# Kernel optimization log

Measured on AMD Instinct MI355X. Metric: run time of the kernel, lower is better.

The kernel has to match this reference:

```python
import jax, jax.numpy as jnp
import numpy as np

DIM = 256
HEADS = 8
HD = DIM // HEADS        # head_dim = 32
WS = 8                   # window_size (Wh = Ww = 8)
NEXP = 8                 # num_experts
HID = 128                # attr_hidden_size (router hidden)
SCALE = HD ** -0.5


def _window_partition(x, ws):
    # (B, H, W, C) -> (B * H//ws * W//ws, ws, ws, C)
    B, H, W, C = x.shape
    x = x.reshape(B, H // ws, ws, W // ws, ws, C)
    return x.transpose(0, 1, 3, 2, 4, 5).reshape(-1, ws, ws, C)


def _window_reverse(w, ws, B, H, W):
    # inverse of _window_partition
    C = w.shape[-1]
    x = w.reshape(B, H // ws, W // ws, ws, ws, C)
    return x.transpose(0, 1, 3, 2, 4, 5).reshape(B, H, W, C)


def _rope2(x):
    # 2D rotary embedding over a window: x (B*, Wh, Ww, d).
    # First d/2 channels rotated by row position, last d/2 by column position.
    B, Wh, Ww, d = x.shape
    d2 = d // 2

    def angles(L, dd):
        inv = 1.0 / (10000.0 ** (jnp.arange(0, dd, 2, dtype=jnp.float32) / dd))
        return jnp.arange(L, dtype=jnp.float32)[:, None] * inv[None, :]  # (L, dd//2)

    def rotate(v, ang, bshape):
        # v: (B, Wh, Ww, dd) pairs interleaved; ang broadcast as bshape
        p = v.reshape(*v.shape[:-1], -1, 2)
        c = jnp.cos(ang).reshape(bshape)
        s = jnp.sin(ang).reshape(bshape)
        o0 = p[..., 0] * c - p[..., 1] * s
        o1 = p[..., 0] * s + p[..., 1] * c
        return jnp.stack([o0, o1], axis=-1).reshape(v.shape)

    ah = angles(Wh, d2)  # (Wh, d2//2)
    aw = angles(Ww, d2)  # (Ww, d2//2)
    xh = rotate(x[..., :d2], ah, (1, Wh, 1, d2 // 2))
    xw = rotate(x[..., d2:], aw, (1, 1, Ww, d2 // 2))
    return jnp.concatenate([xh, xw], axis=-1)


def _moe_linear(xf, routes, w, b):
    # Top-1 dispatch: per-expert dense GEMM, masked select (jit-safe, static shapes).
    # xf: (T, in), routes: (T,) int, w: (E, out, in), b: (E, out)
    out = jnp.zeros((xf.shape[0], w.shape[1]), xf.dtype)
    for i in range(w.shape[0]):
        y = xf @ w[i].T + b[i]
        out = jnp.where((routes == i)[:, None], y, out)
    return out


def setup_inputs() -> dict:
    key = jax.random.key(0)
    ks = jax.random.split(key, 8)
    sc = 0.02
    return {
        "x": jax.random.normal(ks[0], (8, 64, 64, DIM), jnp.float32),
        "router_w1": jax.random.normal(ks[1], (HID, DIM), jnp.float32) * sc,
        "router_b1": jnp.zeros((HID,), jnp.float32),
        "router_w2": jax.random.normal(ks[2], (NEXP, HID), jnp.float32) * sc,
        "router_b2": jnp.zeros((NEXP,), jnp.float32),
        "qkv_w": jax.random.normal(ks[3], (NEXP, 3 * DIM, DIM), jnp.float32) * sc,
        "qkv_b": jnp.zeros((NEXP, 3 * DIM), jnp.float32),
        "proj_w": jax.random.normal(ks[4], (NEXP, DIM, DIM), jnp.float32) * sc,
        "proj_b": jnp.zeros((NEXP, DIM), jnp.float32),
    }


def reference(x, router_w1, router_b1, router_w2, router_b2,
              qkv_w, qkv_b, proj_w, proj_b):
    Bs, H, W, C = x.shape
    xf = x.reshape(-1, C)  # (T, C), T = Bs*H*W

    # --- Top-1 router (eval mode: no noise, no token dropping) ---
    h = jax.nn.relu(xf @ router_w1.T + router_b1)
    router_logits = h @ router_w2.T + router_b2          # (T, E)
    router_probs = jax.nn.softmax(router_logits, axis=-1)
    route_prob_max = jnp.max(router_probs, axis=-1)       # (T,)
    routes = jnp.argmax(router_probs, axis=-1)            # (T,)

    # --- per-expert QKV projection (grouped dispatch) ---
    qkv = _moe_linear(xf, routes, qkv_w, qkv_b)           # (T, 3C)
    qkv = qkv.reshape(Bs, H, W, 3 * C)

    # --- window partition (shift=0, dilated=1 -> no roll, mask=None) ---
    qw = _window_partition(qkv, WS).reshape(-1, WS * WS, 3 * C)
    B_, N, _ = qw.shape
    qkv5 = qw.reshape(B_, N, 3, HEADS, HD).transpose(2, 0, 3, 1, 4)  # (3,B_,h,N,hd)
    q, k, v = qkv5[0], qkv5[1], qkv5[2]

    # --- RoPE on q, k over the 2D window ---
    q = _rope2(q.reshape(-1, WS, WS, HD)).reshape(B_, HEADS, N, HD)
    k = _rope2(k.reshape(-1, WS, WS, HD)).reshape(B_, HEADS, N, HD)

    # --- windowed attention (moe_mask is all zeros in eval: no drops) ---
    attn = jax.nn.softmax((q * SCALE) @ k.swapaxes(-2, -1), axis=-1)  # (B_,h,N,N)
    out = (attn @ v).swapaxes(1, 2).reshape(B_, N, C)

    # --- window reverse ---
    out = _window_reverse(out.reshape(-1, WS, WS, C), WS, Bs, H, W)

    # --- per-expert output projection + Switch-style prob scaling ---
    of = _moe_linear(out.reshape(-1, C), routes, proj_w, proj_b)
    of = of * route_prob_max[:, None]
    return of.reshape(Bs, H, W, C)
```

## Files before the change

kernel.cpp:

```cpp
#include <hip/hip_runtime.h>
#include <hip/hip_bf16.h>

typedef unsigned short u16;
typedef unsigned int u32;
typedef __attribute__((ext_vector_type(8))) short short8;
typedef __attribute__((ext_vector_type(4))) float f32x4;

#define T_TOK 32768
#define SCALE_ATT 0.17677669529663687f

__device__ __forceinline__ u16 f2bf(float f){
  u32 u = __float_as_uint(f);
  u32 r = u + 0x7fffu + ((u >> 16) & 1u);
  return (u16)(r >> 16);
}
__device__ __forceinline__ float bf2f(u16 h){
  return __uint_as_float(((u32)h) << 16);
}

__global__ void k_cvt(const float* __restrict__ s, u16* __restrict__ d, int n4){
  int i = blockIdx.x * blockDim.x + threadIdx.x;
  if (i < n4){
    float4 v = ((const float4*)s)[i];
    ushort4 o;
    o.x = f2bf(v.x); o.y = f2bf(v.y); o.z = f2bf(v.z); o.w = f2bf(v.w);
    ((ushort4*)d)[i] = o;
  }
}

__global__ void k_cvt_split(const float* __restrict__ s, u16* __restrict__ hi,
                            u16* __restrict__ lo, int n){
  int i = blockIdx.x * blockDim.x + threadIdx.x;
  if (i < n){
    float v = s[i];
    u16 h = f2bf(v);
    hi[i] = h;
    lo[i] = f2bf(v - bf2f(h));
  }
}

__global__ void k_init(int* counts, int* cursors){
  int t = threadIdx.x;
  if (t < 8){ counts[t] = 0; cursors[t] = 0; }
}

__global__ __launch_bounds__(256) void k_router(
    const float* __restrict__ x, const u16* __restrict__ w1h, const u16* __restrict__ w1l,
    const float* __restrict__ b1, const float* __restrict__ w2, const float* __restrict__ b2,
    int* __restrict__ routes, float* __restrict__ pmax, int* __restrict__ counts,
    u16* __restrict__ x_bf)
{
  __shared__ __align__(16) char smem[64*132*4];
  u16* Ah = (u16*)smem;
  u16* Al = Ah + 2560;
  u16* Bh = Al + 2560;
  u16* Bl = Bh + 5120;
  float* Hs = (float*)smem;
  __shared__ int lhist[8];

  int tid = threadIdx.x;
  int t0 = blockIdx.x * 64;
  int wv = tid >> 6, lane = tid & 63, quad = lane >> 4, l16 = lane & 15;
  if (tid < 8) lhist[tid] = 0;

  int arow = tid >> 2, acg = tid & 3;
  int brow = tid >> 1, bhalf = tid & 1;

  f32x4 acc[4][2];
  #pragma unroll
  for (int i = 0; i < 4; ++i)
    #pragma unroll
    for (int j = 0; j < 2; ++j)
      #pragma unroll
      for (int rr = 0; rr < 4; ++rr) acc[i][j][rr] = 0.f;

  for (int kt = 0; kt < 8; ++kt){
    const float* gx = x + (size_t)(t0 + arow) * 256 + kt * 32 + acg * 8;
    float4 v0 = *(const float4*)gx;
    float4 v1 = *(const float4*)(gx + 4);
    ushort4 h0, h1, l0, l1;
    h0.x = f2bf(v0.x); h0.y = f2bf(v0.y); h0.z = f2bf(v0.z); h0.w = f2bf(v0.w);
    h1.x = f2bf(v1.x); h1.y = f2bf(v1.y); h1.z = f2bf(v1.z); h1.w = f2bf(v1.w);
    l0.x = f2bf(v0.x - bf2f(h0.x)); l0.y = f2bf(v0.y - bf2f(h0.y));
    l0.z = f2bf(v0.z - bf2f(h0.z)); l0.w = f2bf(v0.w - bf2f(h0.w));
    l1.x = f2bf(v1.x - bf2f(h1.x)); l1.y = f2bf(v1.y - bf2f(h1.y));
    l1.z = f2bf(v1.z - bf2f(h1.z)); l1.w = f2bf(v1.w - bf2f(h1.w));
    u16* gxb = x_bf + (size_t)(t0 + arow) * 256 + kt * 32 + acg * 8;
    *(ushort4*)gxb = h0; *(ushort4*)(gxb + 4) = h1;
    const u16* gwh = w1h + (size_t)brow * 256 + kt * 32 + bhalf * 16;
    const u16* gwl = w1l + (size_t)brow * 256 + kt * 32 + bhalf * 16;
    uint4 wh0 = *(const uint4*)gwh;
    uint4 wh1 = *(const uint4*)(gwh + 8);
    uint4 wl0 = *(const uint4*)gwl;
    uint4 wl1 = *(const uint4*)(gwl + 8);
    __syncthreads();
    *(ushort4*)&Ah[arow*40 + acg*8    ] = h0;
    *(ushort4*)&Ah[arow*40 + acg*8 + 4] = h1;
    *(ushort4*)&Al[arow*40 + acg*8    ] = l0;
    *(ushort4*)&Al[arow*40 + acg*8 + 4] = l1;
    *(uint4*)&Bh[brow*40 + bhalf*16    ] = wh0;
    *(uint4*)&Bh[brow*40 + bhalf*16 + 8] = wh1;
    *(uint4*)&Bl[brow*40 + bhalf*16    ] = wl0;
    *(uint4*)&Bl[brow*40 + bhalf*16 + 8] = wl1;
    __syncthreads();
    short8 ah[4], al[4], bhf[2], blf[2];
    #pragma unroll
    for (int i = 0; i < 4; ++i){
      ah[i] = *(const short8*)&Ah[(i*16 + l16)*40 + quad*8];
      al[i] = *(const short8*)&Al[(i*16 + l16)*40 + quad*8];
    }
    #pragma unroll
    for (int j = 0; j < 2; ++j){
      bhf[j] = *(const short8*)&Bh[(wv*32 + j*16 + l16)*40 + quad*8];
      blf[j] = *(const short8*)&Bl[(wv*32 + j*16 + l16)*40 + quad*8];
    }
    #pragma unroll
    for (int i = 0; i < 4; ++i)
      #pragma unroll
      for (int j = 0; j < 2; ++j){
        acc[i][j] = __builtin_amdgcn_mfma_f32_16x16x32_bf16(ah[i], bhf[j], acc[i][j], 0, 0, 0);
        acc[i][j] = __builtin_amdgcn_mfma_f32_16x16x32_bf16(ah[i], blf[j], acc[i][j], 0, 0, 0);
        acc[i][j] = __builtin_amdgcn_mfma_f32_16x16x32_bf16(al[i], bhf[j], acc[i][j], 0, 0, 0);
      }
  }
  __syncthreads();

  #pragma unroll
  for (int i = 0; i < 4; ++i)
    #pragma unroll
    for (int j = 0; j < 2; ++j){
      int col = wv*32 + j*16 + l16;
      float bb = b1[col];
      #pragma unroll
      for (int rr = 0; rr < 4; ++rr){
        float h = acc[i][j][rr] + bb;
        Hs[(i*16 + quad*4 + rr)*132 + col] = h > 0.f ? h : 0.f;
      }
    }
  __syncthreads();

  #pragma unroll
  for (int pass = 0; pass < 2; ++pass){
    int mtok = (tid >> 3) + pass * 32;
    int e = tid & 7;
    const float4* w2r = (const float4*)(w2 + e * 128);
    float l = b2[e];
    #pragma unroll
    for (int k4 = 0; k4 < 32; ++k4){
      float4 w = w2r[k4];
      int k = k4 * 4;
      l = fmaf(Hs[mtok*132+k  ], w.x, l);
      l = fmaf(Hs[mtok*132+k+1], w.y, l);
      l = fmaf(Hs[mtok*132+k+2], w.z, l);
      l = fmaf(Hs[mtok*132+k+3], w.w, l);
    }
    float mv = l; int mi = e;
    #pragma unroll
    for (int off = 1; off < 8; off <<= 1){
      float ov = __shfl_xor(mv, off, 64);
      int   oi = __shfl_xor(mi, off, 64);
      if (ov > mv || (ov == mv && oi < mi)){ mv = ov; mi = oi; }
    }
    float sum = expf(l - mv);
    #pragma unroll
    for (int off = 1; off < 8; off <<= 1) sum += __shfl_xor(sum, off, 64);
    if (e == 0){
      int t = t0 + mtok;
      routes[t] = mi;
      pmax[t] = 1.0f / sum;
      atomicAdd(&lhist[mi], 1);
    }
  }
  __syncthreads();
  if (tid < 8 && lhist[tid] > 0) atomicAdd(&counts[tid], lhist[tid]);
}

__global__ void k_offsets(const int* __restrict__ counts, int* __restrict__ offs,
                          int* __restrict__ sorted){
  __shared__ int so[9];
  if (threadIdx.x == 0){
    int o = 0; so[0] = 0;
    for (int e = 0; e < 8; ++e){ o += ((counts[e] + 127) >> 7) << 7; so[e+1] = o; }
    for (int e = 0; e < 9; ++e) offs[e] = so[e];
  }
  __syncthreads();
  for (int e = 0; e < 8; ++e){
    int s = so[e] + counts[e], en = so[e+1];
    for (int i = s + (int)threadIdx.x; i < en; i += (int)blockDim.x) sorted[i] = -1;
  }
}

__global__ __launch_bounds__(256) void k_scatter(
    const int* __restrict__ routes, const int* __restrict__ offs,
    int* __restrict__ cursors, int* __restrict__ sorted)
{
  __shared__ int lc[8], lb[8];
  int tid = threadIdx.x;
  int t = blockIdx.x * 256 + tid;
  if (tid < 8) lc[tid] = 0;
  __syncthreads();
  int e = routes[t];
  int rank = atomicAdd(&lc[e], 1);
  __syncthreads();
  if (tid < 8 && lc[tid] > 0) lb[tid] = atomicAdd(&cursors[tid], lc[tid]);
  __syncthreads();
  sorted[offs[e] + lb[e] + rank] = t;
}

#define ASTR 56
template<int NOUT, bool PROJ>
__global__ __launch_bounds__(256) void k_gemm(
    const u16* __restrict__ A, const u16* __restrict__ W,
    const float* __restrict__ bias, const int* __restrict__ sidx,
    const int* __restrict__ offs, const float* __restrict__ pmax,
    u16* __restrict__ outb, float* __restrict__ outf)
{
  __shared__ __align__(16) u16 As[128 * ASTR];
  __shared__ __align__(16) u16 Bs[128 * ASTR];
  int tid = threadIdx.x;
  int m0 = blockIdx.y * 128;
  int n0 = blockIdx.x * 128;
  int total = offs[8];
  if (m0 >= total) return;
  int e = 0;
  #pragma unroll
  for (int i = 1; i < 8; ++i) if (m0 >= offs[i]) e = i;

  int wv = tid >> 6, lane = tid & 63, quad = lane >> 4, l16 = lane & 15;
  int wrow = (wv >> 1) * 64, wcol = (wv & 1) * 64;

  int sm = tid & 127, part = tid >> 7;
  int tokA = sidx[m0 + sm];
  const u16* arow = A + (size_t)(tokA < 0 ? 0 : tokA) * 256 + part * 16;
  int rb = tid & 127;
  int r64 = rb & 63;
  int bcol = n0 + (rb >> 6) * 64 + (r64 >> 4) + (r64 & 15) * 4;
  const u16* brow = W + ((size_t)e * NOUT + bcol) * 256 + part * 16;

  f32x4 acc[4][4];
  #pragma unroll
  for (int i = 0; i < 4; ++i)
    #pragma unroll
    for (int j = 0; j < 4; ++j)
      #pragma unroll
      for (int r = 0; r < 4; ++r) acc[i][j][r] = 0.f;

  uint4 a0 = ((const uint4*)arow)[0], a1 = ((const uint4*)arow)[1];
  uint4 b0 = ((const uint4*)brow)[0], b1 = ((const uint4*)brow)[1];
  if (tokA < 0){ a0.x=a0.y=a0.z=a0.w=0u; a1.x=a1.y=a1.z=a1.w=0u; }

  for (int kt = 0; kt < 8; ++kt){
    __syncthreads();
    *(uint4*)&As[sm*ASTR + part*16    ] = a0;
    *(uint4*)&As[sm*ASTR + part*16 + 8] = a1;
    *(uint4*)&Bs[rb*ASTR + part*16    ] = b0;
    *(uint4*)&Bs[rb*ASTR + part*16 + 8] = b1;
    __syncthreads();
    if (kt < 7){
      const uint4* ga = (const uint4*)(arow + (kt+1) * 32);
      a0 = ga[0]; a1 = ga[1];
      if (tokA < 0){ a0.x=a0.y=a0.z=a0.w=0u; a1.x=a1.y=a1.z=a1.w=0u; }
      const uint4* gb = (const uint4*)(brow + (kt+1) * 32);
      b0 = gb[0]; b1 = gb[1];
    }
    short8 af[4], bfv[4];
    #pragma unroll
    for (int i = 0; i < 4; ++i)
      af[i] = *(const short8*)&As[(wrow + i*16 + l16)*ASTR + quad*8];
    #pragma unroll
    for (int j = 0; j < 4; ++j)
      bfv[j] = *(const short8*)&Bs[(wcol + j*16 + l16)*ASTR + quad*8];
    #pragma unroll
    for (int i = 0; i < 4; ++i)
      #pragma unroll
      for (int j = 0; j < 4; ++j)
        acc[i][j] = __builtin_amdgcn_mfma_f32_16x16x32_bf16(af[i], bfv[j], acc[i][j], 0, 0, 0);
  }

  float4 bj4 = *(const float4*)&bias[e*NOUT + n0 + wcol + l16*4];
  #pragma unroll
  for (int i = 0; i < 4; ++i){
    #pragma unroll
    for (int ri = 0; ri < 4; ++ri){
      int row = wrow + i*16 + quad*4 + ri;
      int t = sidx[m0 + row];
      if (t < 0) continue;
      if (PROJ){
        float pm = pmax[t];
        float4 ov;
        ov.x = (acc[i][0][ri] + bj4.x) * pm;
        ov.y = (acc[i][1][ri] + bj4.y) * pm;
        ov.z = (acc[i][2][ri] + bj4.z) * pm;
        ov.w = (acc[i][3][ri] + bj4.w) * pm;
        *(float4*)&outf[(size_t)t * NOUT + n0 + wcol + l16*4] = ov;
      } else {
        uint2 ov;
        ov.x = (u32)f2bf(acc[i][0][ri] + bj4.x) | ((u32)f2bf(acc[i][1][ri] + bj4.y) << 16);
        ov.y = (u32)f2bf(acc[i][2][ri] + bj4.z) | ((u32)f2bf(acc[i][3][ri] + bj4.w) << 16);
        *(uint2*)&outb[(size_t)t * NOUT + n0 + wcol + l16*4] = ov;
      }
    }
  }
}

__global__ __launch_bounds__(128) void k_attn(const u16* __restrict__ qkv,
                                              u16* __restrict__ attn)
{
  __shared__ __align__(16) u16 lds[2][8576];
  int tid = threadIdx.x;
  int w = tid >> 6, lane = tid & 63;
  u16* Qs = &lds[w][0];
  u16* Ks = &lds[w][2560];
  u16* Ps = &lds[w][0];
  u16* Vt = &lds[w][5120];

  int wh = blockIdx.x * 2 + w;
  if (wh >= 4096) return;
  int win = wh >> 3, head = wh & 7;
  int b = win >> 6, wy = (win >> 3) & 7, wx = win & 7;
  int r = lane >> 3, c = lane & 7;
  int tn = b * 4096 + (wy*8 + r) * 64 + (wx*8 + c);
  const u16* base = qkv + (size_t)tn * 768 + head * 32;

  uint4 qa[4], ka[4], va[4];
  #pragma unroll
  for (int i = 0; i < 4; ++i){
    qa[i] = ((const uint4*)(base      ))[i];
    ka[i] = ((const uint4*)(base + 256))[i];
    va[i] = ((const uint4*)(base + 512))[i];
  }
  u32* qu = (u32*)qa; u32* ku = (u32*)ka; u32* vu = (u32*)va;

  #pragma unroll
  for (int j = 0; j < 8; ++j){
    float inv = __expf(-1.1512925465f * (float)j);
    float ah = (float)r * inv, aw = (float)c * inv;
    float ch = cosf(ah), sh = sinf(ah), cw = cosf(aw), sw = sinf(aw);
    u32 v0, v1; float a0, b0;
    v0 = qu[j];   a0 = bf2f((u16)(v0 & 0xffff)); b0 = bf2f((u16)(v0 >> 16));
    qu[j]   = (u32)f2bf(a0*ch - b0*sh) | ((u32)f2bf(a0*sh + b0*ch) << 16);
    v1 = qu[8+j]; a0 = bf2f((u16)(v1 & 0xffff)); b0 = bf2f((u16)(v1 >> 16));
    qu[8+j] = (u32)f2bf(a0*cw - b0*sw) | ((u32)f2bf(a0*sw + b0*cw) << 16);
    v0 = ku[j];   a0 = bf2f((u16)(v0 & 0xffff)); b0 = bf2f((u16)(v0 >> 16));
    ku[j]   = (u32)f2bf(a0*ch - b0*sh) | ((u32)f2bf(a0*sh + b0*ch) << 16);
    v1 = ku[8+j]; a0 = bf2f((u16)(v1 & 0xffff)); b0 = bf2f((u16)(v1 >> 16));
    ku[8+j] = (u32)f2bf(a0*cw - b0*sw) | ((u32)f2bf(a0*sw + b0*cw) << 16);
  }

  #pragma unroll
  for (int i = 0; i < 4; ++i){
    *(uint4*)&Qs[lane*40 + i*8] = qa[i];
    *(uint4*)&Ks[lane*40 + i*8] = ka[i];
  }
  int pn = (lane & 15) * 4 + (lane >> 4);
  #pragma unroll
  for (int d2 = 0; d2 < 16; ++d2){
    Vt[(2*d2  )*72 + pn] = (u16)(vu[d2] & 0xffff);
    Vt[(2*d2+1)*72 + pn] = (u16)(vu[d2] >> 16);
  }
  uint4 ones = {0x3F803F80u, 0x3F803F80u, 0x3F803F80u, 0x3F803F80u};
  *(uint4*)&Vt[(32 + (lane >> 3))*72 + (lane & 7)*8] = ones;
  *(uint4*)&Vt[(40 + (lane >> 3))*72 + (lane & 7)*8] = ones;

  int quad = lane >> 4, l16 = lane & 15;

  short8 qf[4], kf[4];
  #pragma unroll
  for (int i = 0; i < 4; ++i) qf[i] = *(const short8*)&Qs[(i*16 + l16)*40 + quad*8];
  #pragma unroll
  for (int j = 0; j < 4; ++j) kf[j] = *(const short8*)&Ks[(j*16 + l16)*40 + quad*8];

  f32x4 sa[4][4];
  #pragma unroll
  for (int i = 0; i < 4; ++i)
    #pragma unroll
    for (int j = 0; j < 4; ++j){
      #pragma unroll
      for (int rr = 0; rr < 4; ++rr) sa[i][j][rr] = 0.f;
      sa[i][j] = __builtin_amdgcn_mfma_f32_16x16x32_bf16(qf[i], kf[j], sa[i][j], 0, 0, 0);
    }

  #pragma unroll
  for (int i = 0; i < 4; ++i)
    #pragma unroll
    for (int rr = 0; rr < 4; ++rr){
      float e0 = __expf(sa[i][0][rr] * SCALE_ATT);
      float e1 = __expf(sa[i][1][rr] * SCALE_ATT);
      float e2 = __expf(sa[i][2][rr] * SCALE_ATT);
      float e3 = __expf(sa[i][3][rr] * SCALE_ATT);
      uint2 pk;
      pk.x = (u32)f2bf(e0) | ((u32)f2bf(e1) << 16);
      pk.y = (u32)f2bf(e2) | ((u32)f2bf(e3) << 16);
      *(uint2*)&Ps[(i*16 + quad*4 + rr)*72 + l16*4] = pk;
    }

  f32x4 oa[4][2], os[4];
  #pragma unroll
  for (int i = 0; i < 4; ++i){
    #pragma unroll
    for (int rr = 0; rr < 4; ++rr){ oa[i][0][rr] = 0.f; oa[i][1][rr] = 0.f; os[i][rr] = 0.f; }
  }
  #pragma unroll
  for (int ks = 0; ks < 2; ++ks){
    short8 vf0 = *(const short8*)&Vt[(     l16)*72 + ks*32 + quad*8];
    short8 vf1 = *(const short8*)&Vt[(16 + l16)*72 + ks*32 + quad*8];
    short8 vf2 = *(const short8*)&Vt[(32 + l16)*72 + ks*32 + quad*8];
    #pragma unroll
    for (int i = 0; i < 4; ++i){
      short8 pf = *(const short8*)&Ps[(i*16 + l16)*72 + ks*32 + quad*8];
      oa[i][0] = __builtin_amdgcn_mfma_f32_16x16x32_bf16(pf, vf0, oa[i][0], 0, 0, 0);
      oa[i][1] = __builtin_amdgcn_mfma_f32_16x16x32_bf16(pf, vf1, oa[i][1], 0, 0, 0);
      os[i]    = __builtin_amdgcn_mfma_f32_16x16x32_bf16(pf, vf2, os[i],    0, 0, 0);
    }
  }

  int tb = b * 4096 + wy * 512 + wx * 8;
  #pragma unroll
  for (int i = 0; i < 4; ++i)
    #pragma unroll
    for (int rr = 0; rr < 4; ++rr){
      float inv = __builtin_amdgcn_rcpf(os[i][rr]);
      int m = i*16 + quad*4 + rr;
      int tm = tb + (m >> 3) * 64 + (m & 7);
      u16* op = attn + (size_t)tm * 256 + head * 32 + l16;
      op[0]  = f2bf(oa[i][0][rr] * inv);
      op[16] = f2bf(oa[i][1][rr] * inv);
    }
}

extern "C" void kernel_launch(void* const* d_in, const int* in_sizes, int n_in,
                              void* d_out, int out_size, void* d_ws, size_t ws_size,
                              hipStream_t stream){
  const float* x     = (const float*)d_in[0];
  const float* rw1   = (const float*)d_in[1];
  const float* rb1   = (const float*)d_in[2];
  const float* rw2   = (const float*)d_in[3];
  const float* rb2   = (const float*)d_in[4];
  const float* qkvw  = (const float*)d_in[5];
  const float* qkvb  = (const float*)d_in[6];
  const float* projw = (const float*)d_in[7];
  const float* projb = (const float*)d_in[8];
  float* out = (float*)d_out;

  char* ws = (char*)d_ws;
  u16*   x_bf    = (u16*)(ws);
  u16*   qkv_bf  = (u16*)(ws + 16777216);
  u16*   attn_bf = (u16*)(ws + 67108864);
  u16*   qw_bf   = (u16*)(ws + 83886080);
  u16*   pw_bf   = (u16*)(ws + 87031808);
  int*   routes  = (int*)(ws + 88080384);
  float* pmaxp   = (float*)(ws + 88211456);
  int*   sorted  = (int*)(ws + 88342528);
  int*   counts  = (int*)(ws + 88477696);
  int*   cursors = (int*)(ws + 88477696 + 32);
  int*   offs    = (int*)(ws + 88477696 + 64);
  u16*   w1h     = attn_bf;
  u16*   w1l     = attn_bf + 32768;

  k_init<<<1, 64, 0, stream>>>(counts, cursors);
  k_cvt<<<1536, 256, 0, stream>>>(qkvw,  qw_bf, 1572864/4);
  k_cvt<<< 512, 256, 0, stream>>>(projw, pw_bf,  524288/4);
  k_cvt_split<<<128, 256, 0, stream>>>(rw1, w1h, w1l, 32768);
  k_router<<<512, 256, 0, stream>>>(x, w1h, w1l, rb1, rw2, rb2, routes, pmaxp, counts, x_bf);
  k_offsets<<<1, 256, 0, stream>>>(counts, offs, sorted);
  k_scatter<<<128, 256, 0, stream>>>(routes, offs, cursors, sorted);
  k_gemm<768, false><<<dim3(6, 264), 256, 0, stream>>>(x_bf, qw_bf, qkvb, sorted, offs,
                                                       nullptr, qkv_bf, nullptr);
  k_attn<<<2048, 128, 0, stream>>>(qkv_bf, attn_bf);
  k_gemm<256, true><<<dim3(2, 264), 256, 0, stream>>>(attn_bf, pw_bf, projb, sorted, offs,
                                                      pmaxp, nullptr, out);
}
```

Before: 239.8 us.

## Pre-gather routed tokens into expert-sorted contiguous buffers for MoE GEMMs

Adds a gather kernel that copies bf16 tokens into expert-sorted order, and has the attention kernel write its output directly at each token's sorted position via a new rank array. Both GEMMs can then load A tiles with contiguous, coalesced row reads instead of indirect per-row gathers, and the negative-index masking disappears from the GEMM inner loop. The cost is an extra kernel launch plus a full copy of x, and the attention stores become scattered through the rank indirection.

```diff
diff --git a/kernel.cpp b/kernel.cpp
--- a/kernel.cpp
+++ b/kernel.cpp
@@ -192,7 +192,7 @@
 
 __global__ __launch_bounds__(256) void k_scatter(
     const int* __restrict__ routes, const int* __restrict__ offs,
-    int* __restrict__ cursors, int* __restrict__ sorted)
+    int* __restrict__ cursors, int* __restrict__ sorted, int* __restrict__ rank)
 {
   __shared__ int lc[8], lb[8];
   int tid = threadIdx.x;
@@ -200,11 +200,31 @@
   if (tid < 8) lc[tid] = 0;
   __syncthreads();
   int e = routes[t];
-  int rank = atomicAdd(&lc[e], 1);
+  int rl = atomicAdd(&lc[e], 1);
   __syncthreads();
   if (tid < 8 && lc[tid] > 0) lb[tid] = atomicAdd(&cursors[tid], lc[tid]);
   __syncthreads();
-  sorted[offs[e] + lb[e] + rank] = t;
+  int pos = offs[e] + lb[e] + rl;
+  sorted[pos] = t;
+  rank[t] = pos;
+}
+
+__global__ __launch_bounds__(256) void k_gather(
+    const u16* __restrict__ xbf, const int* __restrict__ sorted,
+    const int* __restrict__ offs, u16* __restrict__ xs)
+{
+  int total = offs[8];
+  int tid = threadIdx.x;
+  #pragma unroll
+  for (int h = 0; h < 2; ++h){
+    int cid = tid + h * 256;
+    int row = cid >> 5, chunk = cid & 31;
+    int gr = blockIdx.x * 16 + row;
+    int t = (gr < total) ? sorted[gr] : -1;
+    uint4 v = {0u, 0u, 0u, 0u};
+    if (t >= 0) v = *(const uint4*)(xbf + (size_t)t * 256 + chunk * 8);
+    *(uint4*)(xs + (size_t)gr * 256 + chunk * 8) = v;
+  }
 }
 
 #define ASTR 56
@@ -229,13 +249,12 @@
   int wv = tid >> 6, lane = tid & 63, quad = lane >> 4, l16 = lane & 15;
   int wrow = (wv >> 1) * 64, wcol = (wv & 1) * 64;
 
-  int sm = tid & 127, part = tid >> 7;
-  int tokA = sidx[m0 + sm];
-  const u16* arow = A + (size_t)(tokA < 0 ? 0 : tokA) * 256 + part * 16;
-  int rb = tid & 127;
-  int r64 = rb & 63;
-  int bcol = n0 + (rb >> 6) * 64 + (r64 >> 4) + (r64 & 15) * 4;
-  const u16* brow = W + ((size_t)e * NOUT + bcol) * 256 + part * 16;
+  int row0 = tid >> 2, c0 = tid & 3;
+  const u16* aptr0 = A + (size_t)(m0 + row0) * 256 + c0 * 8;
+  const u16* aptr1 = aptr0 + (size_t)64 * 256;
+  int pc = (row0 >> 4) + (row0 & 15) * 4;
+  const u16* bptr0 = W + ((size_t)e * NOUT + n0 + pc) * 256 + c0 * 8;
+  const u16* bptr1 = W + ((size_t)e * NOUT + n0 + 64 + pc) * 256 + c0 * 8;
 
   f32x4 acc[4][4];
   #pragma unroll
@@ -245,23 +264,21 @@
       #pragma unroll
       for (int r = 0; r < 4; ++r) acc[i][j][r] = 0.f;
 
-  uint4 a0 = ((const uint4*)arow)[0], a1 = ((const uint4*)arow)[1];
-  uint4 b0 = ((const uint4*)brow)[0], b1 = ((const uint4*)brow)[1];
-  if (tokA < 0){ a0.x=a0.y=a0.z=a0.w=0u; a1.x=a1.y=a1.z=a1.w=0u; }
+  uint4 a0 = *(const uint4*)aptr0, a1 = *(const uint4*)aptr1;
+  uint4 b0 = *(const uint4*)bptr0, b1 = *(const uint4*)bptr1;
 
   for (int kt = 0; kt < 8; ++kt){
     __syncthreads();
-    *(uint4*)&As[sm*ASTR + part*16    ] = a0;
-    *(uint4*)&As[sm*ASTR + part*16 + 8] = a1;
-    *(uint4*)&Bs[rb*ASTR + part*16    ] = b0;
-    *(uint4*)&Bs[rb*ASTR + part*16 + 8] = b1;
+    *(uint4*)&As[ row0      *ASTR + c0*8] = a0;
+    *(uint4*)&As[(row0 + 64)*ASTR + c0*8] = a1;
+    *(uint4*)&Bs[ row0      *ASTR + c0*8] = b0;
+    *(uint4*)&Bs[(row0 + 64)*ASTR + c0*8] = b1;
     __syncthreads();
     if (kt < 7){
-      const uint4* ga = (const uint4*)(arow + (kt+1) * 32);
-      a0 = ga[0]; a1 = ga[1];
-      if (tokA < 0){ a0.x=a0.y=a0.z=a0.w=0u; a1.x=a1.y=a1.z=a1.w=0u; }
-      const uint4* gb = (const uint4*)(brow + (kt+1) * 32);
-      b0 = gb[0]; b1 = gb[1];
+      a0 = *(const uint4*)(aptr0 + (kt+1)*32);
+      a1 = *(const uint4*)(aptr1 + (kt+1)*32);
+      b0 = *(const uint4*)(bptr0 + (kt+1)*32);
+      b1 = *(const uint4*)(bptr1 + (kt+1)*32);
     }
     short8 af[4], bfv[4];
     #pragma unroll
@@ -304,7 +321,8 @@
 }
 
 __global__ __launch_bounds__(128) void k_attn(const u16* __restrict__ qkv,
-                                              u16* __restrict__ attn)
+                                              const int* __restrict__ rank,
+                                              u16* __restrict__ attn_s)
 {
   __shared__ __align__(16) u16 lds[2][8576];
   int tid = threadIdx.x;
@@ -422,7 +440,8 @@
       float inv = __builtin_amdgcn_rcpf(os[i][rr]);
       int m = i*16 + quad*4 + rr;
       int tm = tb + (m >> 3) * 64 + (m & 7);
-      u16* op = attn + (size_t)tm * 256 + head * 32 + l16;
+      int pos = rank[tm];
+      u16* op = attn_s + (size_t)pos * 256 + head * 32 + l16;
       op[0]  = f2bf(oa[i][0][rr] * inv);
       op[16] = f2bf(oa[i][1][rr] * inv);
     }
@@ -445,17 +464,19 @@
   char* ws = (char*)d_ws;
   u16*   x_bf    = (u16*)(ws);
   u16*   qkv_bf  = (u16*)(ws + 16777216);
-  u16*   attn_bf = (u16*)(ws + 67108864);
-  u16*   qw_bf   = (u16*)(ws + 83886080);
-  u16*   pw_bf   = (u16*)(ws + 87031808);
-  int*   routes  = (int*)(ws + 88080384);
-  float* pmaxp   = (float*)(ws + 88211456);
-  int*   sorted  = (int*)(ws + 88342528);
-  int*   counts  = (int*)(ws + 88477696);
-  int*   cursors = (int*)(ws + 88477696 + 32);
-  int*   offs    = (int*)(ws + 88477696 + 64);
-  u16*   w1h     = attn_bf;
-  u16*   w1l     = attn_bf + 32768;
+  u16*   w1h     = (u16*)(ws + 67108864);
+  u16*   w1l     = w1h + 32768;
+  u16*   xs      = (u16*)(ws + 67108864);
+  u16*   attn_s  = (u16*)(ws + 67108864);
+  u16*   qw_bf   = (u16*)(ws + 84410368);
+  u16*   pw_bf   = (u16*)(ws + 87556096);
+  int*   routes  = (int*)(ws + 88604672);
+  float* pmaxp   = (float*)(ws + 88735744);
+  int*   sorted  = (int*)(ws + 88866816);
+  int*   rank    = (int*)(ws + 89001984);
+  int*   counts  = (int*)(ws + 89133056);
+  int*   cursors = (int*)(ws + 89133056 + 32);
+  int*   offs    = (int*)(ws + 89133056 + 64);
 
   k_init<<<1, 64, 0, stream>>>(counts, cursors);
   k_cvt<<<1536, 256, 0, stream>>>(qkvw,  qw_bf, 1572864/4);
@@ -463,10 +484,11 @@
   k_cvt_split<<<128, 256, 0, stream>>>(rw1, w1h, w1l, 32768);
   k_router<<<512, 256, 0, stream>>>(x, w1h, w1l, rb1, rw2, rb2, routes, pmaxp, counts, x_bf);
   k_offsets<<<1, 256, 0, stream>>>(counts, offs, sorted);
-  k_scatter<<<128, 256, 0, stream>>>(routes, offs, cursors, sorted);
-  k_gemm<768, false><<<dim3(6, 264), 256, 0, stream>>>(x_bf, qw_bf, qkvb, sorted, offs,
+  k_scatter<<<128, 256, 0, stream>>>(routes, offs, cursors, sorted, rank);
+  k_gather<<<2112, 256, 0, stream>>>(x_bf, sorted, offs, xs);
+  k_gemm<768, false><<<dim3(6, 264), 256, 0, stream>>>(xs, qw_bf, qkvb, sorted, offs,
                                                        nullptr, qkv_bf, nullptr);
-  k_attn<<<2048, 128, 0, stream>>>(qkv_bf, attn_bf);
-  k_gemm<256, true><<<dim3(2, 264), 256, 0, stream>>>(attn_bf, pw_bf, projb, sorted, offs,
+  k_attn<<<2048, 128, 0, stream>>>(qkv_bf, rank, attn_s);
+  k_gemm<256, true><<<dim3(2, 264), 256, 0, stream>>>(attn_s, pw_bf, projb, sorted, offs,
                                                       pmaxp, nullptr, out);
 }
```

After: 225.6 us. 5.9% less time.
